# Optimization experiments

Hardware: AMD Instinct MI355X
Metric: run time of the kernel (lower is better)

The kernel has to match this reference:

```python
import jax, jax.numpy as jnp
import numpy as np

N = 100000      # nodes
E = 1600000     # edges (before self loops)
IN_DIM, EMB, HID, OUT, L = 128, 128, 128, 64, 3
LN_EPS = 1e-5


def _lin(k, fi, fo):
    return (jax.random.normal(k, (fi, fo), jnp.float32) / np.sqrt(fi)).astype(jnp.float32)


def setup_inputs() -> dict:
    key = jax.random.key(0)
    ks = jax.random.split(key, 8)
    x = jax.random.normal(ks[0], (N, IN_DIM), jnp.float32)
    edge_index = jax.random.randint(ks[1], (2, E), 0, N, dtype=jnp.int64)
    # in-degree of destination nodes (as data.degree would provide)
    degree = jnp.zeros((N,), jnp.float32).at[edge_index[1]].add(1.0)
    lks = jax.random.split(ks[2], 2 * L)
    W1 = jnp.stack([_lin(lks[2 * i], EMB, HID) for i in range(L)])
    W2 = jnp.stack([_lin(lks[2 * i + 1], HID, EMB) for i in range(L)])
    return dict(
        x=x, edge_index=edge_index, degree=degree,
        Win=_lin(ks[3], IN_DIM, EMB), b_in=jnp.zeros((EMB,), jnp.float32),
        W1=W1, b1=jnp.zeros((L, HID), jnp.float32),
        W2=W2, b2=jnp.zeros((L, EMB), jnp.float32),
        ln_g=jnp.ones((L, EMB), jnp.float32), ln_b=jnp.zeros((L, EMB), jnp.float32),
        out_g=jnp.ones((EMB,), jnp.float32), out_b=jnp.zeros((EMB,), jnp.float32),
        Wout=_lin(ks[4], EMB, OUT), b_out=jnp.zeros((OUT,), jnp.float32),
    )


def _layernorm(h, g, b):
    m = h.mean(-1, keepdims=True)
    v = ((h - m) ** 2).mean(-1, keepdims=True)
    return (h - m) * jax.lax.rsqrt(v + LN_EPS) * g + b


def reference(x, edge_index, degree, Win, b_in, W1, b1, W2, b2,
              ln_g, ln_b, out_g, out_b, Wout, b_out):
    # input_lin: Linear -> Dropout(eval: identity) -> ReLU
    h = jax.nn.relu(x @ Win + b_in)                        # [N, EMB]
    # add self loops, degree + 1
    loop = jnp.arange(N, dtype=edge_index.dtype)
    src = jnp.concatenate([edge_index[0], loop])           # [E+N]
    dst = jnp.concatenate([edge_index[1], loop])
    inv = jax.lax.rsqrt(degree + 1.0)                      # deg^{-1/2}
    coef = (inv[src] * inv[dst])[:, None]                  # symmetric GCN norm
    for i in range(L):
        m = h @ W1[i] + b1[i]                              # [N, HID]
        agg = jax.ops.segment_sum(m[src] * coef, dst, num_segments=N)  # gather-scatter
        out = agg @ W2[i] + b2[i]                          # [N, EMB]
        h = jax.nn.relu(_layernorm(out + h, ln_g[i], ln_b[i]))  # residual + LN + act (dropout=id)
    h = _layernorm(h, out_g, out_b)
    return h @ Wout + b_out
```

## Files before the change

kernel.cpp:

```cpp
#include <hip/hip_runtime.h>
#include <cstdint>
#include <cstddef>

typedef unsigned short u16;
typedef unsigned int u32;
typedef __attribute__((ext_vector_type(2))) unsigned short u16x2;
typedef __attribute__((ext_vector_type(4))) unsigned short u16x4;
typedef __attribute__((ext_vector_type(8))) unsigned short u16x8;
typedef __attribute__((ext_vector_type(8))) __bf16 bf16x8;
typedef __attribute__((ext_vector_type(4))) float f32x4;

#define PREP_F32   0
#define PREP_BF16  1
#define PREP_LN    2
#define EPI_IN    0
#define EPI_SCALE 1
#define EPI_NONE  3

__device__ __forceinline__ float wred(float v) {
#pragma unroll
  for (int m = 32; m >= 1; m >>= 1) v += __shfl_xor(v, m, 64);
  return v;
}
__device__ __forceinline__ u16 f2bf(float f) {
  u32 u = __float_as_uint(f);
  u += 0x7fffu + ((u >> 16) & 1u);
  return (u16)(u >> 16);
}
__device__ __forceinline__ float bflo(u32 u) { return __uint_as_float(u << 16); }
__device__ __forceinline__ float bfhi(u32 u) { return __uint_as_float(u & 0xffff0000u); }
__device__ __forceinline__ u32 pack2(float a, float b) {
  u32 ua = __float_as_uint(a); ua += 0x7fffu + ((ua >> 16) & 1u);
  u32 ub = __float_as_uint(b); ub += 0x7fffu + ((ub >> 16) & 1u);
  return (ua >> 16) | (ub & 0xffff0000u);
}

__global__ void scan_block_k(const float* __restrict__ deg, int* __restrict__ offs,
                             int* __restrict__ bsum, int N) {
  __shared__ int sh[256];
  int tid = threadIdx.x;
  int i = blockIdx.x * 256 + tid;
  int c = (i < N) ? (int)(deg[i] + 0.5f) : 0;
  int val = c;
  for (int off = 1; off < 256; off <<= 1) {
    sh[tid] = val; __syncthreads();
    if (tid >= off) val += sh[tid - off];
    __syncthreads();
  }
  if (i < N) offs[i] = val - c;
  if (tid == 255) bsum[blockIdx.x] = val;
}

__global__ void scan_bsum_k(int* __restrict__ bsum, int nb) {
  __shared__ int sh[1024];
  int tid = threadIdx.x;
  int c = (tid < nb) ? bsum[tid] : 0;
  int val = c;
  for (int off = 1; off < 1024; off <<= 1) {
    sh[tid] = val; __syncthreads();
    if (tid >= off) val += sh[tid - off];
    __syncthreads();
  }
  if (tid < nb) bsum[tid] = val - c;
}

__global__ void scan_add_k(int* __restrict__ offs, const int* __restrict__ bsum,
                           int* __restrict__ gcur, float* __restrict__ inv,
                           const float* __restrict__ deg, int N, int E) {
  int i = blockIdx.x * 256 + threadIdx.x;
  if (i < N) {
    int o = offs[i] + bsum[i >> 8];
    offs[i] = o;
    inv[i] = rsqrtf(deg[i] + 1.0f);
    if ((i & 511) == 0) gcur[i >> 9] = o;
  } else if (i == N) {
    offs[N] = E;
  }
}

__global__ __launch_bounds__(256) void scatter_k(
    const int* __restrict__ src, const int* __restrict__ dst,
    int* __restrict__ gcur, u32* __restrict__ pairs, int E) {
  __shared__ int hist[256];
  __shared__ int base_[256];
  const int tid = threadIdx.x;
  const int e0 = blockIdx.x * 8192;
  const int e1 = min(E, e0 + 8192);
  hist[tid] = 0;
  __syncthreads();
  for (int e = e0 + tid; e < e1; e += 256)
    atomicAdd(&hist[dst[e] >> 9], 1);
  __syncthreads();
  int c = hist[tid];
  if (c > 0) base_[tid] = atomicAdd(&gcur[tid], c);
  hist[tid] = 0;
  __syncthreads();
  for (int e = e0 + tid; e < e1; e += 256) {
    int d = dst[e];
    int b = d >> 9;
    int r = atomicAdd(&hist[b], 1);
    pairs[base_[b] + r] = (u32)src[e] | ((u32)(d & 511) << 17);
  }
}

__global__ __launch_bounds__(256) void fill2_k(
    const u32* __restrict__ pairs, const int* __restrict__ offs,
    int* __restrict__ col, int N) {
  __shared__ int cur[512];
  const int b = blockIdx.x;
  const int n0 = b << 9;
  const int n1 = min(N, n0 + 512);
  const int tid = threadIdx.x;
  for (int i = tid; i < n1 - n0; i += 256) cur[i] = offs[n0 + i];
  __syncthreads();
  const int e0 = offs[n0], e1 = offs[n1];
  for (int e = e0 + tid; e < e1; e += 256) {
    u32 pr = pairs[e];
    int p = atomicAdd(&cur[pr >> 17], 1);
    col[p] = (int)(pr & 0x1FFFFu);
  }
}

__global__ void pack_all_k(const float* __restrict__ Win, const float* __restrict__ W1,
                           const float* __restrict__ W2, const float* __restrict__ Wout,
                           u16* __restrict__ pWin, u16* __restrict__ pW1,
                           u16* __restrict__ pW2, u16* __restrict__ pWout) {
  const int b = blockIdx.x;
  const float* W; u16* P; int ncol; int t;
  if (b < 8)       { W = Win;                        P = pWin;                      ncol = 128; t = b * 256 + threadIdx.x; }
  else if (b < 32) { int l = (b - 8) / 8;  W = W1 + (size_t)l * 16384;  P = pW1 + (size_t)l * 16384; ncol = 128; t = ((b - 8) % 8) * 256 + threadIdx.x; }
  else if (b < 56) { int l = (b - 32) / 8; W = W2 + (size_t)l * 16384;  P = pW2 + (size_t)l * 16384; ncol = 128; t = ((b - 32) % 8) * 256 + threadIdx.x; }
  else             { W = Wout;                       P = pWout;                     ncol = 64;  t = (b - 56) * 256 + threadIdx.x; }
  int NT = ncol >> 4;
  int total = 4 * NT * 64;
  if (t >= total) return;
  int lane = t & 63;
  int tmp = t >> 6;
  int nt = tmp % NT, kc = tmp / NT;
  int n = nt * 16 + (lane & 15);
  int kb = kc * 32 + ((lane >> 4) << 2);
  u16* dst = P + (size_t)t * 8;
#pragma unroll
  for (int j = 0; j < 8; ++j) {
    int k = kb + (j & 3) + ((j >> 2) << 4);
    dst[j] = f2bf(W[(size_t)k * ncol + n]);
  }
}

__global__ __launch_bounds__(256) void spmm_gemm_k(
    const uint4* __restrict__ msc, const int* __restrict__ offs,
    const int* __restrict__ col, const float* __restrict__ inv,
    const u16* __restrict__ Wp, const float* __restrict__ bias,
    u32* __restrict__ h, const float* __restrict__ g1,
    const float* __restrict__ lb1, int N) {
  __shared__ union {
    u16  xs[32][136];
    float cs[16][132];
  } sh;
  const int tid = threadIdx.x;
  const int lane = tid & 63, wid = tid >> 6;
  const int row0 = blockIdx.x * 32;
  const int rgrp = lane >> 4, c = lane & 15;

#pragma unroll
  for (int p = 0; p < 2; ++p) {
    const int lrow = wid * 8 + p * 4 + rgrp;
    const int d = row0 + lrow;
    const int s0 = offs[d], s1 = offs[d + 1];
    const int last = s1 - 1;
    float2 a0 = {0.f, 0.f}, a1 = {0.f, 0.f}, a2 = {0.f, 0.f}, a3 = {0.f, 0.f};
    for (int k = s0; k < s1; k += 8) {
      int sv[8];
#pragma unroll
      for (int j = 0; j < 8; ++j) sv[j] = col[min(k + j, last)];
      uint4 rv[8];
#pragma unroll
      for (int j = 0; j < 8; ++j) rv[j] = msc[(size_t)sv[j] * 16 + c];
#pragma unroll
      for (int j = 0; j < 8; ++j) {
        float m = (k + j < s1) ? 1.f : 0.f;
        a0.x = fmaf(m, bflo(rv[j].x), a0.x); a0.y = fmaf(m, bfhi(rv[j].x), a0.y);
        a1.x = fmaf(m, bflo(rv[j].y), a1.x); a1.y = fmaf(m, bfhi(rv[j].y), a1.y);
        a2.x = fmaf(m, bflo(rv[j].z), a2.x); a2.y = fmaf(m, bfhi(rv[j].z), a2.y);
        a3.x = fmaf(m, bflo(rv[j].w), a3.x); a3.y = fmaf(m, bfhi(rv[j].w), a3.y);
      }
    }
    uint4 r = msc[(size_t)d * 16 + c];
    float iv = inv[d];
    uint4 o;
    o.x = pack2((a0.x + bflo(r.x)) * iv, (a0.y + bfhi(r.x)) * iv);
    o.y = pack2((a1.x + bflo(r.y)) * iv, (a1.y + bfhi(r.y)) * iv);
    o.z = pack2((a2.x + bflo(r.z)) * iv, (a2.y + bfhi(r.z)) * iv);
    o.w = pack2((a3.x + bflo(r.w)) * iv, (a3.y + bfhi(r.w)) * iv);
    *(uint4*)&sh.xs[lrow][c * 8] = o;
  }
  __syncthreads();

  const int m0  = (wid >> 1) << 4;
  const int ntb = (wid & 1) << 2;
  f32x4 acc[4];
#pragma unroll
  for (int t = 0; t < 4; ++t) acc[t] = (f32x4){0.f, 0.f, 0.f, 0.f};
  const int ar  = m0 + (lane & 15);
  const int akb = (lane >> 4) << 2;
  const bf16x8* Bp = (const bf16x8*)Wp;
#pragma unroll
  for (int kc = 0; kc < 4; ++kc) {
    u16x4 lo = *(const u16x4*)&sh.xs[ar][kc * 32 + akb];
    u16x4 hi = *(const u16x4*)&sh.xs[ar][kc * 32 + akb + 16];
    u16x8 av;
#pragma unroll
    for (int j = 0; j < 4; ++j) { av[j] = lo[j]; av[j + 4] = hi[j]; }
    bf16x8 a = __builtin_bit_cast(bf16x8, av);
#pragma unroll
    for (int t = 0; t < 4; ++t) {
      bf16x8 b = Bp[(kc * 8 + ntb + t) * 64 + lane];
      acc[t] = __builtin_amdgcn_mfma_f32_16x16x32_bf16(a, b, acc[t], 0, 0, 0);
    }
  }

  const int cb = lane & 15;
  const int rg = (lane >> 4) << 2;
  float2 gg = *(const float2*)&g1[lane * 2];
  float2 bb = *(const float2*)&lb1[lane * 2];
#pragma unroll
  for (int hh = 0; hh < 2; ++hh) {
    __syncthreads();
    if ((m0 >> 4) == hh) {
#pragma unroll
      for (int t = 0; t < 4; ++t) {
        int colm = (ntb + t) * 16 + cb;
        float bv = bias[colm];
#pragma unroll
        for (int r = 0; r < 4; ++r) sh.cs[rg + r][colm] = acc[t][r] + bv;
      }
    }
    __syncthreads();
    for (int rr = 0; rr < 4; ++rr) {
      int lr = wid * 4 + rr;
      int gr = row0 + hh * 16 + lr;
      float2 t2 = *(const float2*)&sh.cs[lr][lane * 2];
      u32 hv = h[(size_t)gr * 64 + lane];
      float tx = t2.x + bflo(hv), ty = t2.y + bfhi(hv);
      float mean = wred(tx + ty) * (1.f / 128.f);
      float dx = tx - mean, dy = ty - mean;
      float var = wred(dx * dx + dy * dy) * (1.f / 128.f);
      float rstd = rsqrtf(var + 1e-5f);
      float y0 = fmaxf(dx * rstd * gg.x + bb.x, 0.f);
      float y1 = fmaxf(dy * rstd * gg.y + bb.y, 0.f);
      h[(size_t)gr * 64 + lane] = pack2(y0, y1);
    }
  }
}

template <int NOUT, int PREP, int EPI>
__global__ __launch_bounds__(256) void gemm_mfma(
    const void* __restrict__ Xv, const u16* __restrict__ Wp,
    const float* __restrict__ bias, void* __restrict__ Yv,
    const void* __restrict__ resv,
    const float* __restrict__ g1, const float* __restrict__ lb1,
    int N) {
  constexpr int NT = NOUT / 16;
  __shared__ union {
    u16  xs[32][136];
    float cs[32][132];
  } sh;
  const int tid = threadIdx.x;
  const int lane = tid & 63, wid = tid >> 6;
  const int row0 = blockIdx.x * 32;

  if constexpr (PREP == PREP_F32) {
    const float* X = (const float*)Xv;
    for (int i = tid; i < 1024; i += 256) {
      int r = i >> 5, c4 = i & 31;
      float4 v = ((const float4*)(X + (size_t)(row0 + r) * 128))[c4];
      u16x4 o = {f2bf(v.x), f2bf(v.y), f2bf(v.z), f2bf(v.w)};
      *(u16x4*)&sh.xs[r][c4 * 4] = o;
    }
  } else if constexpr (PREP == PREP_BF16) {
    const u16x4* X = (const u16x4*)Xv;
    for (int i = tid; i < 1024; i += 256) {
      int r = i >> 5, c4 = i & 31;
      *(u16x4*)&sh.xs[r][c4 * 4] = X[(size_t)(row0 + r) * 32 + c4];
    }
  } else {
    const u32* X = (const u32*)Xv;
    float2 gg = *(const float2*)&g1[lane * 2];
    float2 bb = *(const float2*)&lb1[lane * 2];
    for (int rr = 0; rr < 8; ++rr) {
      int r = wid * 8 + rr;
      u32 v = X[(size_t)(row0 + r) * 64 + lane];
      float tx = bflo(v), ty = bfhi(v);
      float mean = wred(tx + ty) * (1.f / 128.f);
      float dx = tx - mean, dy = ty - mean;
      float var = wred(dx * dx + dy * dy) * (1.f / 128.f);
      float rstd = rsqrtf(var + 1e-5f);
      u16x2 o = {f2bf(dx * rstd * gg.x + bb.x), f2bf(dy * rstd * gg.y + bb.y)};
      *(u16x2*)&sh.xs[r][lane * 2] = o;
    }
  }
  __syncthreads();

  constexpr int NTW = (NOUT == 128) ? 4 : 2;
  const int m0  = (NOUT == 128) ? ((wid >> 1) << 4) : ((wid & 1) << 4);
  const int ntb = (NOUT == 128) ? ((wid & 1) << 2) : ((wid >> 1) << 1);

  f32x4 acc[NTW];
#pragma unroll
  for (int t = 0; t < NTW; ++t) acc[t] = (f32x4){0.f, 0.f, 0.f, 0.f};

  const int ar  = m0 + (lane & 15);
  const int akb = (lane >> 4) << 2;
  const bf16x8* Bp = (const bf16x8*)Wp;
#pragma unroll
  for (int kc = 0; kc < 4; ++kc) {
    u16x4 lo = *(const u16x4*)&sh.xs[ar][kc * 32 + akb];
    u16x4 hi = *(const u16x4*)&sh.xs[ar][kc * 32 + akb + 16];
    u16x8 av;
#pragma unroll
    for (int j = 0; j < 4; ++j) { av[j] = lo[j]; av[j + 4] = hi[j]; }
    bf16x8 a = __builtin_bit_cast(bf16x8, av);
#pragma unroll
    for (int t = 0; t < NTW; ++t) {
      bf16x8 b = Bp[(kc * NT + ntb + t) * 64 + lane];
      acc[t] = __builtin_amdgcn_mfma_f32_16x16x32_bf16(a, b, acc[t], 0, 0, 0);
    }
  }

  const int cb = lane & 15;
  const int rg = (lane >> 4) << 2;
  if constexpr (EPI == EPI_NONE) {
    float* Y = (float*)Yv;
#pragma unroll
    for (int t = 0; t < NTW; ++t) {
      int col = (ntb + t) * 16 + cb;
      float bv = bias[col];
#pragma unroll
      for (int r = 0; r < 4; ++r) {
        int gr = row0 + m0 + rg + r;
        Y[(size_t)gr * NOUT + col] = acc[t][r] + bv;
      }
    }
  } else if constexpr (EPI == EPI_SCALE) {
    const float* inv = (const float*)resv;
    u16* Y = (u16*)Yv;
#pragma unroll
    for (int t = 0; t < NTW; ++t) {
      int col = (ntb + t) * 16 + cb;
      float bv = bias[col];
#pragma unroll
      for (int r = 0; r < 4; ++r) {
        int gr = row0 + m0 + rg + r;
        Y[(size_t)gr * NOUT + col] = f2bf((acc[t][r] + bv) * inv[gr]);
      }
    }
  } else {
    __syncthreads();
#pragma unroll
    for (int t = 0; t < NTW; ++t) {
      int col = (ntb + t) * 16 + cb;
      float bv = bias[col];
#pragma unroll
      for (int r = 0; r < 4; ++r) sh.cs[m0 + rg + r][col] = acc[t][r] + bv;
    }
    __syncthreads();
    u32* Y = (u32*)Yv;
    for (int rr = 0; rr < 8; ++rr) {
      int r = wid * 8 + rr;
      int gr = row0 + r;
      float2 t2 = *(const float2*)&sh.cs[r][lane * 2];
      Y[(size_t)gr * 64 + lane] = pack2(fmaxf(t2.x, 0.f), fmaxf(t2.y, 0.f));
    }
  }
}

extern "C" void kernel_launch(void* const* d_in, const int* in_sizes, int n_in,
                              void* d_out, int out_size, void* d_ws, size_t ws_size,
                              hipStream_t stream) {
  (void)n_in; (void)out_size; (void)ws_size;
  const float* x      = (const float*)d_in[0];
  const int*   eidx   = (const int*)d_in[1];
  const float* degree = (const float*)d_in[2];
  const float* Win    = (const float*)d_in[3];
  const float* b_in   = (const float*)d_in[4];
  const float* W1     = (const float*)d_in[5];
  const float* b1     = (const float*)d_in[6];
  const float* W2     = (const float*)d_in[7];
  const float* b2     = (const float*)d_in[8];
  const float* ln_g   = (const float*)d_in[9];
  const float* ln_b   = (const float*)d_in[10];
  const float* out_g  = (const float*)d_in[11];
  const float* out_b  = (const float*)d_in[12];
  const float* Wout   = (const float*)d_in[13];
  const float* b_out  = (const float*)d_in[14];

  const int N = in_sizes[0] / 128;
  const int E = in_sizes[1] / 2;
  const int* esrc = eidx;
  const int* edst = eidx + E;

  char* p = (char*)d_ws;
  auto alloc = [&](size_t bytes) {
    char* q = p;
    p += (bytes + 255) & ~(size_t)255;
    return q;
  };
  float* inv    = (float*)alloc((size_t)N * 4);
  int*   offs   = (int*)alloc(((size_t)N + 1) * 4);
  int*   gcur   = (int*)alloc(256 * 4);
  int*   bsum   = (int*)alloc(1024 * 4);
  int*   col    = (int*)alloc((size_t)E * 4);
  u32*   pairs  = (u32*)alloc((size_t)E * 4);
  u32*   h      = (u32*)alloc((size_t)N * 128 * 2);
  u32*   msc    = (u32*)alloc((size_t)N * 128 * 2);
  u16*   pWin   = (u16*)alloc(4 * 8 * 64 * 8 * 2);
  u16*   pWout  = (u16*)alloc(4 * 4 * 64 * 8 * 2);
  u16*   pW1    = (u16*)alloc(3 * 4 * 8 * 64 * 8 * 2);
  u16*   pW2    = (u16*)alloc(3 * 4 * 8 * 64 * 8 * 2);

  pack_all_k<<<60, 256, 0, stream>>>(Win, W1, W2, Wout, pWin, pW1, pW2, pWout);

  const int nb = (N + 255) / 256;
  const int NB = (N + 511) / 512;
  scan_block_k<<<nb, 256, 0, stream>>>(degree, offs, bsum, N);
  scan_bsum_k<<<1, 1024, 0, stream>>>(bsum, nb);
  scan_add_k<<<(N + 256) / 256, 256, 0, stream>>>(offs, bsum, gcur, inv, degree, N, E);
  scatter_k<<<(E + 8191) / 8192, 256, 0, stream>>>(esrc, edst, gcur, pairs, E);
  fill2_k<<<NB, 256, 0, stream>>>(pairs, offs, col, N);

  const int gemmGrid = (N + 31) / 32;

  gemm_mfma<128, PREP_F32, EPI_IN><<<gemmGrid, 256, 0, stream>>>(
      x, pWin, b_in, h, nullptr, nullptr, nullptr, N);
  for (int l = 0; l < 3; ++l) {
    gemm_mfma<128, PREP_BF16, EPI_SCALE><<<gemmGrid, 256, 0, stream>>>(
        h, pW1 + (size_t)l * 16384, b1 + l * 128, msc, inv, nullptr, nullptr, N);
    spmm_gemm_k<<<gemmGrid, 256, 0, stream>>>(
        (const uint4*)msc, offs, col, inv, pW2 + (size_t)l * 16384,
        b2 + l * 128, h, ln_g + l * 128, ln_b + l * 128, N);
  }
  gemm_mfma<64, PREP_LN, EPI_NONE><<<gemmGrid, 256, 0, stream>>>(
      h, pWout, b_out, d_out, nullptr, out_g, out_b, N);
}
```

Baseline: 370.3 us.

## Merge CSR-build prep kernels into the input and first-layer GEMM launches

Independent setup work is folded into the GEMM launches by giving extra blocks a different role. Degree scan and weight packing share one launch, the block-sum scan rides on the input GEMM, and the scan-add runs alongside the layer-0 W1 GEMM. This cuts the number of kernel launches and lets small serial kernels overlap with GEMM work. The cost is more complex kernels with role-dispatch branches, and the shared-memory union is now sized for the largest role.

```diff
diff --git a/kernel.cpp b/kernel.cpp
--- a/kernel.cpp
+++ b/kernel.cpp
@@ -35,97 +35,152 @@
   return (ua >> 16) | (ub & 0xffff0000u);
 }
 
-__global__ void scan_block_k(const float* __restrict__ deg, int* __restrict__ offs,
-                             int* __restrict__ bsum, int N) {
-  __shared__ int sh[256];
-  int tid = threadIdx.x;
-  int i = blockIdx.x * 256 + tid;
-  int c = (i < N) ? (int)(deg[i] + 0.5f) : 0;
-  int val = c;
-  for (int off = 1; off < 256; off <<= 1) {
-    sh[tid] = val; __syncthreads();
-    if (tid >= off) val += sh[tid - off];
+
+template <int NOUT, int PREP, int EPI>
+__device__ __forceinline__ void gemm_body(
+    const void* __restrict__ Xv, const u16* __restrict__ Wp,
+    const float* __restrict__ bias, void* __restrict__ Yv,
+    const void* __restrict__ resv, const float* __restrict__ g1,
+    const float* __restrict__ lb1, int N, int bid) {
+  constexpr int NT = NOUT / 16;
+  __shared__ union {
+    u16  xs[32][136];
+    float cs[32][132];
+  } sh;
+  const int tid = threadIdx.x;
+  const int lane = tid & 63, wid = tid >> 6;
+  const int row0 = bid * 32;
+
+  if constexpr (PREP == PREP_F32) {
+    const float* X = (const float*)Xv;
+    for (int i = tid; i < 1024; i += 256) {
+      int r = i >> 5, c4 = i & 31;
+      float4 v = ((const float4*)(X + (size_t)(row0 + r) * 128))[c4];
+      u16x4 o = {f2bf(v.x), f2bf(v.y), f2bf(v.z), f2bf(v.w)};
+      *(u16x4*)&sh.xs[r][c4 * 4] = o;
+    }
+  } else if constexpr (PREP == PREP_BF16) {
+    const u16x4* X = (const u16x4*)Xv;
+    for (int i = tid; i < 1024; i += 256) {
+      int r = i >> 5, c4 = i & 31;
+      *(u16x4*)&sh.xs[r][c4 * 4] = X[(size_t)(row0 + r) * 32 + c4];
+    }
+  } else {
+    const u32* X = (const u32*)Xv;
+    float2 gg = *(const float2*)&g1[lane * 2];
+    float2 bb = *(const float2*)&lb1[lane * 2];
+    for (int rr = 0; rr < 8; ++rr) {
+      int r = wid * 8 + rr;
+      u32 v = X[(size_t)(row0 + r) * 64 + lane];
+      float tx = bflo(v), ty = bfhi(v);
+      float mean = wred(tx + ty) * (1.f / 128.f);
+      float dx = tx - mean, dy = ty - mean;
+      float var = wred(dx * dx + dy * dy) * (1.f / 128.f);
+      float rstd = rsqrtf(var + 1e-5f);
+      u16x2 o = {f2bf(dx * rstd * gg.x + bb.x), f2bf(dy * rstd * gg.y + bb.y)};
+      *(u16x2*)&sh.xs[r][lane * 2] = o;
+    }
+  }
+  __syncthreads();
+
+  constexpr int NTW = (NOUT == 128) ? 4 : 2;
+  const int m0  = (NOUT == 128) ? ((wid >> 1) << 4) : ((wid & 1) << 4);
+  const int ntb = (NOUT == 128) ? ((wid & 1) << 2) : ((wid >> 1) << 1);
+
+  f32x4 acc[NTW];
+#pragma unroll
+  for (int t = 0; t < NTW; ++t) acc[t] = (f32x4){0.f, 0.f, 0.f, 0.f};
+
+  const int ar  = m0 + (lane & 15);
+  const int akb = (lane >> 4) << 2;
+  const bf16x8* Bp = (const bf16x8*)Wp;
+#pragma unroll
+  for (int kc = 0; kc < 4; ++kc) {
+    u16x4 lo = *(const u16x4*)&sh.xs[ar][kc * 32 + akb];
+    u16x4 hi = *(const u16x4*)&sh.xs[ar][kc * 32 + akb + 16];
+    u16x8 av;
+#pragma unroll
+    for (int j = 0; j < 4; ++j) { av[j] = lo[j]; av[j + 4] = hi[j]; }
+    bf16x8 a = __builtin_bit_cast(bf16x8, av);
+#pragma unroll
+    for (int t = 0; t < NTW; ++t) {
+      bf16x8 b = Bp[(kc * NT + ntb + t) * 64 + lane];
+      acc[t] = __builtin_amdgcn_mfma_f32_16x16x32_bf16(a, b, acc[t], 0, 0, 0);
+    }
+  }
+
+  const int cb = lane & 15;
+  const int rg = (lane >> 4) << 2;
+  if constexpr (EPI == EPI_NONE) {
+    float* Y = (float*)Yv;
+#pragma unroll
+    for (int t = 0; t < NTW; ++t) {
+      int col = (ntb + t) * 16 + cb;
+      float bv = bias[col];
+#pragma unroll
+      for (int r = 0; r < 4; ++r) {
+        int gr = row0 + m0 + rg + r;
+        Y[(size_t)gr * NOUT + col] = acc[t][r] + bv;
+      }
+    }
+  } else if constexpr (EPI == EPI_SCALE) {
+    const float* inv = (const float*)resv;
+    u16* Y = (u16*)Yv;
+#pragma unroll
+    for (int t = 0; t < NTW; ++t) {
+      int col = (ntb + t) * 16 + cb;
+      float bv = bias[col];
+#pragma unroll
+      for (int r = 0; r < 4; ++r) {
+        int gr = row0 + m0 + rg + r;
+        Y[(size_t)gr * NOUT + col] = f2bf((acc[t][r] + bv) * inv[gr]);
+      }
+    }
+  } else {
     __syncthreads();
-  }
-  if (i < N) offs[i] = val - c;
-  if (tid == 255) bsum[blockIdx.x] = val;
-}
-
-__global__ void scan_bsum_k(int* __restrict__ bsum, int nb) {
-  __shared__ int sh[1024];
-  int tid = threadIdx.x;
-  int c = (tid < nb) ? bsum[tid] : 0;
-  int val = c;
-  for (int off = 1; off < 1024; off <<= 1) {
-    sh[tid] = val; __syncthreads();
-    if (tid >= off) val += sh[tid - off];
+#pragma unroll
+    for (int t = 0; t < NTW; ++t) {
+      int col = (ntb + t) * 16 + cb;
+      float bv = bias[col];
+#pragma unroll
+      for (int r = 0; r < 4; ++r) sh.cs[m0 + rg + r][col] = acc[t][r] + bv;
+    }
     __syncthreads();
-  }
-  if (tid < nb) bsum[tid] = val - c;
-}
-
-__global__ void scan_add_k(int* __restrict__ offs, const int* __restrict__ bsum,
-                           int* __restrict__ gcur, float* __restrict__ inv,
-                           const float* __restrict__ deg, int N, int E) {
-  int i = blockIdx.x * 256 + threadIdx.x;
-  if (i < N) {
-    int o = offs[i] + bsum[i >> 8];
-    offs[i] = o;
-    inv[i] = rsqrtf(deg[i] + 1.0f);
-    if ((i & 511) == 0) gcur[i >> 9] = o;
-  } else if (i == N) {
-    offs[N] = E;
-  }
-}
-
-__global__ __launch_bounds__(256) void scatter_k(
-    const int* __restrict__ src, const int* __restrict__ dst,
-    int* __restrict__ gcur, u32* __restrict__ pairs, int E) {
-  __shared__ int hist[256];
-  __shared__ int base_[256];
-  const int tid = threadIdx.x;
-  const int e0 = blockIdx.x * 8192;
-  const int e1 = min(E, e0 + 8192);
-  hist[tid] = 0;
-  __syncthreads();
-  for (int e = e0 + tid; e < e1; e += 256)
-    atomicAdd(&hist[dst[e] >> 9], 1);
-  __syncthreads();
-  int c = hist[tid];
-  if (c > 0) base_[tid] = atomicAdd(&gcur[tid], c);
-  hist[tid] = 0;
-  __syncthreads();
-  for (int e = e0 + tid; e < e1; e += 256) {
-    int d = dst[e];
-    int b = d >> 9;
-    int r = atomicAdd(&hist[b], 1);
-    pairs[base_[b] + r] = (u32)src[e] | ((u32)(d & 511) << 17);
-  }
-}
-
-__global__ __launch_bounds__(256) void fill2_k(
-    const u32* __restrict__ pairs, const int* __restrict__ offs,
-    int* __restrict__ col, int N) {
-  __shared__ int cur[512];
-  const int b = blockIdx.x;
-  const int n0 = b << 9;
-  const int n1 = min(N, n0 + 512);
-  const int tid = threadIdx.x;
-  for (int i = tid; i < n1 - n0; i += 256) cur[i] = offs[n0 + i];
-  __syncthreads();
-  const int e0 = offs[n0], e1 = offs[n1];
-  for (int e = e0 + tid; e < e1; e += 256) {
-    u32 pr = pairs[e];
-    int p = atomicAdd(&cur[pr >> 17], 1);
-    col[p] = (int)(pr & 0x1FFFFu);
-  }
-}
-
-__global__ void pack_all_k(const float* __restrict__ Win, const float* __restrict__ W1,
-                           const float* __restrict__ W2, const float* __restrict__ Wout,
-                           u16* __restrict__ pWin, u16* __restrict__ pW1,
-                           u16* __restrict__ pW2, u16* __restrict__ pWout) {
-  const int b = blockIdx.x;
+    u32* Y = (u32*)Yv;
+    for (int rr = 0; rr < 8; ++rr) {
+      int r = wid * 8 + rr;
+      int gr = row0 + r;
+      float2 t2 = *(const float2*)&sh.cs[r][lane * 2];
+      Y[(size_t)gr * 64 + lane] = pack2(fmaxf(t2.x, 0.f), fmaxf(t2.y, 0.f));
+    }
+  }
+}
+
+
+__global__ __launch_bounds__(256) void d1_scan_pack_k(
+    const float* __restrict__ deg, int* __restrict__ offs,
+    int* __restrict__ bsum, float* __restrict__ inv, int N, int nb,
+    const float* __restrict__ Win, const float* __restrict__ W1,
+    const float* __restrict__ W2, const float* __restrict__ Wout,
+    u16* __restrict__ pWin, u16* __restrict__ pW1,
+    u16* __restrict__ pW2, u16* __restrict__ pWout) {
+  if ((int)blockIdx.x < nb) {
+    __shared__ int sh[256];
+    int tid = threadIdx.x;
+    int i = blockIdx.x * 256 + tid;
+    int c = (i < N) ? (int)(deg[i] + 0.5f) : 0;
+    if (i < N) inv[i] = rsqrtf(deg[i] + 1.0f);
+    int val = c;
+    for (int off = 1; off < 256; off <<= 1) {
+      sh[tid] = val; __syncthreads();
+      if (tid >= off) val += sh[tid - off];
+      __syncthreads();
+    }
+    if (i < N) offs[i] = val - c;
+    if (tid == 255) bsum[blockIdx.x] = val;
+    return;
+  }
+  const int b = blockIdx.x - nb;
   const float* W; u16* P; int ncol; int t;
   if (b < 8)       { W = Win;                        P = pWin;                      ncol = 128; t = b * 256 + threadIdx.x; }
   else if (b < 32) { int l = (b - 8) / 8;  W = W1 + (size_t)l * 16384;  P = pW1 + (size_t)l * 16384; ncol = 128; t = ((b - 8) % 8) * 256 + threadIdx.x; }
@@ -147,6 +202,102 @@
   }
 }
 
+__global__ __launch_bounds__(256) void d2_gemmin_bsum_k(
+    const void* __restrict__ Xv, const u16* __restrict__ Wp,
+    const float* __restrict__ bias, void* __restrict__ Yv, int N,
+    int* __restrict__ bsum, int nb) {
+  if (blockIdx.x == gridDim.x - 1) {
+    __shared__ int a[512], b[512];
+    int tid = threadIdx.x;
+    for (int i = tid; i < 512; i += 256) a[i] = (i < nb) ? bsum[i] : 0;
+    __syncthreads();
+    int* src = a; int* dst = b;
+    for (int off = 1; off < 512; off <<= 1) {
+      for (int i = tid; i < 512; i += 256)
+        dst[i] = (i >= off) ? src[i] + src[i - off] : src[i];
+      __syncthreads();
+      int* t = src; src = dst; dst = t;
+    }
+    for (int i = tid; i < nb; i += 256) bsum[i] = (i > 0) ? src[i - 1] : 0;
+    return;
+  }
+  gemm_body<128, PREP_F32, EPI_IN>(Xv, Wp, bias, Yv, nullptr, nullptr, nullptr,
+                                   N, blockIdx.x);
+}
+
+__global__ __launch_bounds__(256) void d3_gemmscale_scanadd_k(
+    const void* __restrict__ Xv, const u16* __restrict__ Wp,
+    const float* __restrict__ bias, void* __restrict__ Yv,
+    const float* __restrict__ inv, int N,
+    int* __restrict__ offs, const int* __restrict__ bsum,
+    int* __restrict__ gcur, int E, int gemmGrid) {
+  if ((int)blockIdx.x >= gemmGrid) {
+    int i = (blockIdx.x - gemmGrid) * 256 + threadIdx.x;
+    if (i < N) {
+      int o = offs[i] + bsum[i >> 8];
+      offs[i] = o;
+      if ((i & 511) == 0) gcur[i >> 9] = o;
+    } else if (i == N) {
+      offs[N] = E;
+    }
+    return;
+  }
+  gemm_body<128, PREP_BF16, EPI_SCALE>(Xv, Wp, bias, Yv, inv, nullptr, nullptr,
+                                       N, blockIdx.x);
+}
+
+template <int NOUT, int PREP, int EPI>
+__global__ __launch_bounds__(256) void gemm_mfma(
+    const void* __restrict__ Xv, const u16* __restrict__ Wp,
+    const float* __restrict__ bias, void* __restrict__ Yv,
+    const void* __restrict__ resv, const float* __restrict__ g1,
+    const float* __restrict__ lb1, int N) {
+  gemm_body<NOUT, PREP, EPI>(Xv, Wp, bias, Yv, resv, g1, lb1, N, blockIdx.x);
+}
+
+__global__ __launch_bounds__(256) void scatter_k(
+    const int* __restrict__ src, const int* __restrict__ dst,
+    int* __restrict__ gcur, u32* __restrict__ pairs, int E) {
+  __shared__ int hist[256];
+  __shared__ int base_[256];
+  const int tid = threadIdx.x;
+  const int e0 = blockIdx.x * 8192;
+  const int e1 = min(E, e0 + 8192);
+  hist[tid] = 0;
+  __syncthreads();
+  for (int e = e0 + tid; e < e1; e += 256)
+    atomicAdd(&hist[dst[e] >> 9], 1);
+  __syncthreads();
+  int c = hist[tid];
+  if (c > 0) base_[tid] = atomicAdd(&gcur[tid], c);
+  hist[tid] = 0;
+  __syncthreads();
+  for (int e = e0 + tid; e < e1; e += 256) {
+    int d = dst[e];
+    int b = d >> 9;
+    int r = atomicAdd(&hist[b], 1);
+    pairs[base_[b] + r] = (u32)src[e] | ((u32)(d & 511) << 17);
+  }
+}
+
+__global__ __launch_bounds__(256) void fill2_k(
+    const u32* __restrict__ pairs, const int* __restrict__ offs,
+    int* __restrict__ col, int N) {
+  __shared__ int cur[512];
+  const int b = blockIdx.x;
+  const int n0 = b << 9;
+  const int n1 = min(N, n0 + 512);
+  const int tid = threadIdx.x;
+  for (int i = tid; i < n1 - n0; i += 256) cur[i] = offs[n0 + i];
+  __syncthreads();
+  const int e0 = offs[n0], e1 = offs[n1];
+  for (int e = e0 + tid; e < e1; e += 256) {
+    u32 pr = pairs[e];
+    int p = atomicAdd(&cur[pr >> 17], 1);
+    col[p] = (int)(pr & 0x1FFFFu);
+  }
+}
+
 __global__ __launch_bounds__(256) void spmm_gemm_k(
     const uint4* __restrict__ msc, const int* __restrict__ offs,
     const int* __restrict__ col, const float* __restrict__ inv,
@@ -249,127 +400,6 @@
       float y0 = fmaxf(dx * rstd * gg.x + bb.x, 0.f);
       float y1 = fmaxf(dy * rstd * gg.y + bb.y, 0.f);
       h[(size_t)gr * 64 + lane] = pack2(y0, y1);
-    }
-  }
-}
-
-template <int NOUT, int PREP, int EPI>
-__global__ __launch_bounds__(256) void gemm_mfma(
-    const void* __restrict__ Xv, const u16* __restrict__ Wp,
-    const float* __restrict__ bias, void* __restrict__ Yv,
-    const void* __restrict__ resv,
-    const float* __restrict__ g1, const float* __restrict__ lb1,
-    int N) {
-  constexpr int NT = NOUT / 16;
-  __shared__ union {
-    u16  xs[32][136];
-    float cs[32][132];
-  } sh;
-  const int tid = threadIdx.x;
-  const int lane = tid & 63, wid = tid >> 6;
-  const int row0 = blockIdx.x * 32;
-
-  if constexpr (PREP == PREP_F32) {
-    const float* X = (const float*)Xv;
-    for (int i = tid; i < 1024; i += 256) {
-      int r = i >> 5, c4 = i & 31;
-      float4 v = ((const float4*)(X + (size_t)(row0 + r) * 128))[c4];
-      u16x4 o = {f2bf(v.x), f2bf(v.y), f2bf(v.z), f2bf(v.w)};
-      *(u16x4*)&sh.xs[r][c4 * 4] = o;
-    }
-  } else if constexpr (PREP == PREP_BF16) {
-    const u16x4* X = (const u16x4*)Xv;
-    for (int i = tid; i < 1024; i += 256) {
-      int r = i >> 5, c4 = i & 31;
-      *(u16x4*)&sh.xs[r][c4 * 4] = X[(size_t)(row0 + r) * 32 + c4];
-    }
-  } else {
-    const u32* X = (const u32*)Xv;
-    float2 gg = *(const float2*)&g1[lane * 2];
-    float2 bb = *(const float2*)&lb1[lane * 2];
-    for (int rr = 0; rr < 8; ++rr) {
-      int r = wid * 8 + rr;
-      u32 v = X[(size_t)(row0 + r) * 64 + lane];
-      float tx = bflo(v), ty = bfhi(v);
-      float mean = wred(tx + ty) * (1.f / 128.f);
-      float dx = tx - mean, dy = ty - mean;
-      float var = wred(dx * dx + dy * dy) * (1.f / 128.f);
-      float rstd = rsqrtf(var + 1e-5f);
-      u16x2 o = {f2bf(dx * rstd * gg.x + bb.x), f2bf(dy * rstd * gg.y + bb.y)};
-      *(u16x2*)&sh.xs[r][lane * 2] = o;
-    }
-  }
-  __syncthreads();
-
-  constexpr int NTW = (NOUT == 128) ? 4 : 2;
-  const int m0  = (NOUT == 128) ? ((wid >> 1) << 4) : ((wid & 1) << 4);
-  const int ntb = (NOUT == 128) ? ((wid & 1) << 2) : ((wid >> 1) << 1);
-
-  f32x4 acc[NTW];
-#pragma unroll
-  for (int t = 0; t < NTW; ++t) acc[t] = (f32x4){0.f, 0.f, 0.f, 0.f};
-
-  const int ar  = m0 + (lane & 15);
-  const int akb = (lane >> 4) << 2;
-  const bf16x8* Bp = (const bf16x8*)Wp;
-#pragma unroll
-  for (int kc = 0; kc < 4; ++kc) {
-    u16x4 lo = *(const u16x4*)&sh.xs[ar][kc * 32 + akb];
-    u16x4 hi = *(const u16x4*)&sh.xs[ar][kc * 32 + akb + 16];
-    u16x8 av;
-#pragma unroll
-    for (int j = 0; j < 4; ++j) { av[j] = lo[j]; av[j + 4] = hi[j]; }
-    bf16x8 a = __builtin_bit_cast(bf16x8, av);
-#pragma unroll
-    for (int t = 0; t < NTW; ++t) {
-      bf16x8 b = Bp[(kc * NT + ntb + t) * 64 + lane];
-      acc[t] = __builtin_amdgcn_mfma_f32_16x16x32_bf16(a, b, acc[t], 0, 0, 0);
-    }
-  }
-
-  const int cb = lane & 15;
-  const int rg = (lane >> 4) << 2;
-  if constexpr (EPI == EPI_NONE) {
-    float* Y = (float*)Yv;
-#pragma unroll
-    for (int t = 0; t < NTW; ++t) {
-      int col = (ntb + t) * 16 + cb;
-      float bv = bias[col];
-#pragma unroll
-      for (int r = 0; r < 4; ++r) {
-        int gr = row0 + m0 + rg + r;
-        Y[(size_t)gr * NOUT + col] = acc[t][r] + bv;
-      }
-    }
-  } else if constexpr (EPI == EPI_SCALE) {
-    const float* inv = (const float*)resv;
-    u16* Y = (u16*)Yv;
-#pragma unroll
-    for (int t = 0; t < NTW; ++t) {
-      int col = (ntb + t) * 16 + cb;
-      float bv = bias[col];
-#pragma unroll
-      for (int r = 0; r < 4; ++r) {
-        int gr = row0 + m0 + rg + r;
-        Y[(size_t)gr * NOUT + col] = f2bf((acc[t][r] + bv) * inv[gr]);
-      }
-    }
-  } else {
-    __syncthreads();
-#pragma unroll
-    for (int t = 0; t < NTW; ++t) {
-      int col = (ntb + t) * 16 + cb;
-      float bv = bias[col];
-#pragma unroll
-      for (int r = 0; r < 4; ++r) sh.cs[m0 + rg + r][col] = acc[t][r] + bv;
-    }
-    __syncthreads();
-    u32* Y = (u32*)Yv;
-    for (int rr = 0; rr < 8; ++rr) {
-      int r = wid * 8 + rr;
-      int gr = row0 + r;
-      float2 t2 = *(const float2*)&sh.cs[r][lane * 2];
-      Y[(size_t)gr * 64 + lane] = pack2(fmaxf(t2.x, 0.f), fmaxf(t2.y, 0.f));
     }
   }
 }
@@ -418,21 +448,24 @@
   u16*   pW1    = (u16*)alloc(3 * 4 * 8 * 64 * 8 * 2);
   u16*   pW2    = (u16*)alloc(3 * 4 * 8 * 64 * 8 * 2);
 
-  pack_all_k<<<60, 256, 0, stream>>>(Win, W1, W2, Wout, pWin, pW1, pW2, pWout);
-
   const int nb = (N + 255) / 256;
   const int NB = (N + 511) / 512;
-  scan_block_k<<<nb, 256, 0, stream>>>(degree, offs, bsum, N);
-  scan_bsum_k<<<1, 1024, 0, stream>>>(bsum, nb);
-  scan_add_k<<<(N + 256) / 256, 256, 0, stream>>>(offs, bsum, gcur, inv, degree, N, E);
+  const int gemmGrid = (N + 31) / 32;
+  const int saGrid = (N + 256) / 256;
+
+  d1_scan_pack_k<<<nb + 60, 256, 0, stream>>>(
+      degree, offs, bsum, inv, N, nb,
+      Win, W1, W2, Wout, pWin, pW1, pW2, pWout);
+  d2_gemmin_bsum_k<<<gemmGrid + 1, 256, 0, stream>>>(
+      x, pWin, b_in, h, N, bsum, nb);
+  d3_gemmscale_scanadd_k<<<gemmGrid + saGrid, 256, 0, stream>>>(
+      h, pW1, b1, msc, inv, N, offs, bsum, gcur, E, gemmGrid);
   scatter_k<<<(E + 8191) / 8192, 256, 0, stream>>>(esrc, edst, gcur, pairs, E);
   fill2_k<<<NB, 256, 0, stream>>>(pairs, offs, col, N);
 
-  const int gemmGrid = (N + 31) / 32;
-
-  gemm_mfma<128, PREP_F32, EPI_IN><<<gemmGrid, 256, 0, stream>>>(
-      x, pWin, b_in, h, nullptr, nullptr, nullptr, N);
-  for (int l = 0; l < 3; ++l) {
+  spmm_gemm_k<<<gemmGrid, 256, 0, stream>>>(
+      (const uint4*)msc, offs, col, inv, pW2, b2, h, ln_g, ln_b, N);
+  for (int l = 1; l < 3; ++l) {
     gemm_mfma<128, PREP_BF16, EPI_SCALE><<<gemmGrid, 256, 0, stream>>>(
         h, pW1 + (size_t)l * 16384, b1 + l * 128, msc, inv, nullptr, nullptr, N);
     spmm_gemm_k<<<gemmGrid, 256, 0, stream>>>(
```

Result: faster. 362.7 us (-2.0%).
